# Kernel optimization log

Hardware: AMD Instinct MI355X
Metric: run time of the kernel (lower is better)

## Reference

```python
import jax, jax.numpy as jnp
import numpy as np


def setup_inputs() -> dict:
    key = jax.random.key(0)
    ks = jax.random.split(key, 9)
    B, T, C, H = 4, 2048, 1024, 16
    hd = C // H  # 64
    s = 0.02
    return {
        "x": jax.random.normal(ks[0], (B, T, C), dtype=jnp.float32),
        "Wq": jax.random.normal(ks[1], (H, C, hd), dtype=jnp.float32) * s,
        "bq": jax.random.normal(ks[2], (H, hd), dtype=jnp.float32) * s,
        "Wk": jax.random.normal(ks[3], (H, C, hd), dtype=jnp.float32) * s,
        "bk": jax.random.normal(ks[4], (H, hd), dtype=jnp.float32) * s,
        "Wv": jax.random.normal(ks[5], (H, C, hd), dtype=jnp.float32) * s,
        "bv": jax.random.normal(ks[6], (H, hd), dtype=jnp.float32) * s,
        "Wp": jax.random.normal(ks[7], (C, C), dtype=jnp.float32) * s,
        "bp": jax.random.normal(ks[8], (C,), dtype=jnp.float32) * s,
    }


def reference(x, Wq, bq, Wk, bk, Wv, bv, Wp, bp):
    B, T, C = x.shape
    # per-head projections, batched over heads: [B,H,T,hd]
    q = jnp.einsum('btc,hcd->bhtd', x, Wq) + bq[None, :, None, :]
    k = jnp.einsum('btc,hcd->bhtd', x, Wk) + bk[None, :, None, :]
    v = jnp.einsum('btc,hcd->bhtd', x, Wv) + bv[None, :, None, :]
    # NOTE: original scales by full embed dim C (not head_size) -- faithful quirk
    scale = jnp.asarray(C, x.dtype) ** -0.5
    wei = jnp.einsum('bhtd,bhsd->bhts', q, k) * scale  # [B,H,T,T]
    causal = jnp.tril(jnp.ones((T, T), dtype=bool))
    wei = jnp.where(causal, wei, jnp.asarray(-jnp.inf, wei.dtype))
    wei = jax.nn.softmax(wei, axis=-1)
    out = jnp.einsum('bhts,bhsd->bhtd', wei, v)  # [B,H,T,hd]
    # concat heads along feature dim -> [B,T,C]
    out = out.transpose(0, 2, 1, 3).reshape(B, T, C)
    return out @ Wp + bp
```

## Files before the change

### kernel.cpp

```cpp
#include <hip/hip_runtime.h>
#include <hip/hip_bf16.h>
#include <stdint.h>


typedef unsigned short u16;
typedef __attribute__((ext_vector_type(4))) float f32x4;
typedef __attribute__((ext_vector_type(8))) __bf16 bf16x8;
typedef __attribute__((ext_vector_type(2))) __bf16 bf16x2;

#define DEV static __device__ __forceinline__

DEV u16 f2bf(float f) {
  uint32_t u = __builtin_bit_cast(uint32_t, f);
  return (u16)((u + 0x7FFFu + ((u >> 16) & 1u)) >> 16);
}

DEV uint pack2(float a, float b) {
  bf16x2 v;
  v.x = (__bf16)a;
  v.y = (__bf16)b;
  return __builtin_bit_cast(uint, v);
}

#if __has_builtin(__builtin_amdgcn_exp2f)
DEV float fexp2(float x) { return __builtin_amdgcn_exp2f(x); }
#else
DEV float fexp2(float x) { return __expf(x * 0.69314718056f); }
#endif

DEV void gload_lds16(const void* g, void* lds) {
  auto gp = reinterpret_cast<const __attribute__((address_space(1))) uint32_t*>(
      reinterpret_cast<uintptr_t>(g));
  auto lp = reinterpret_cast<__attribute__((address_space(3))) uint32_t*>(
      static_cast<uint32_t>(reinterpret_cast<uintptr_t>(lds)));
  __builtin_amdgcn_global_load_lds(gp, lp, 16, 0, 0);
}

DEV f32x4 mfma16(bf16x8 a, bf16x8 b, f32x4 c) {
  return __builtin_amdgcn_mfma_f32_16x16x32_bf16(a, b, c, 0, 0, 0);
}

DEV void bar() {
  asm volatile("" ::: "memory");
  __builtin_amdgcn_s_barrier();
  asm volatile("" ::: "memory");
}

#define LD8(p) (*reinterpret_cast<const bf16x8*>(p))
#define LDU4(p) (*reinterpret_cast<const uint4*>(p))


__global__ void cvt_x_kernel(const float* __restrict__ x, u16* __restrict__ xb, int n8) {
  int i = blockIdx.x * blockDim.x + threadIdx.x;
  int stride = gridDim.x * blockDim.x;
  for (; i < n8; i += stride) {
    const float4* xp = reinterpret_cast<const float4*>(x) + 2 * (size_t)i;
    float4 a = xp[0], b = xp[1];
    uint4 o;
    o.x = pack2(a.x, a.y);
    o.y = pack2(a.z, a.w);
    o.z = pack2(b.x, b.y);
    o.w = pack2(b.z, b.w);
    reinterpret_cast<uint4*>(xb)[i] = o;
  }
}

__global__ void cvt_wqkv_kernel(const float* __restrict__ Wq, const float* __restrict__ Wk,
                                const float* __restrict__ Wv, const float* __restrict__ bq,
                                const float* __restrict__ bk, const float* __restrict__ bv,
                                u16* __restrict__ wt, float* __restrict__ biasq) {
  __shared__ u16 tle[64 * 72];
  const int tid = threadIdx.x;
  const int ct = blockIdx.x;
  const int h = blockIdx.y;
  const int which = blockIdx.z;
  const float* W = (which == 0) ? Wq : (which == 1) ? Wk : Wv;
  const float* Bb = (which == 0) ? bq : (which == 1) ? bk : bv;
  const float scl = (which == 0) ? 0.045084220027780106f : 1.0f;
#pragma unroll
  for (int i = 0; i < 4; ++i) {
    int idx = i * 256 + tid;
    int c_l = idx >> 4, d4 = (idx & 15) * 4;
    float4 v = *reinterpret_cast<const float4*>(&W[((size_t)(h * 1024 + ct * 64 + c_l)) * 64 + d4]);
    tle[(d4 + 0) * 72 + c_l] = f2bf(v.x * scl);
    tle[(d4 + 1) * 72 + c_l] = f2bf(v.y * scl);
    tle[(d4 + 2) * 72 + c_l] = f2bf(v.z * scl);
    tle[(d4 + 3) * 72 + c_l] = f2bf(v.w * scl);
  }
  __syncthreads();
#pragma unroll
  for (int i = 0; i < 2; ++i) {
    int idx = i * 256 + tid;
    int d_o = idx >> 3, c8 = (idx & 7) * 8;
    uint4 v = LDU4(&tle[d_o * 72 + c8]);
    *reinterpret_cast<uint4*>(&wt[(size_t)(which * 1024 + h * 64 + d_o) * 1024 + ct * 64 + c8]) = v;
  }
  if (ct == 0 && tid < 64) biasq[which * 1024 + h * 64 + tid] = Bb[h * 64 + tid] * scl;
}

__global__ void cvt_wp_kernel(const float* __restrict__ Wp, u16* __restrict__ wpt) {
  __shared__ u16 tle[64 * 72];
  const int tid = threadIdx.x;
  const int ct = blockIdx.x;
  const int nt = blockIdx.y;
#pragma unroll
  for (int i = 0; i < 4; ++i) {
    int idx = i * 256 + tid;
    int c_l = idx >> 4, n4 = (idx & 15) * 4;
    float4 v = *reinterpret_cast<const float4*>(&Wp[(size_t)(ct * 64 + c_l) * 1024 + nt * 64 + n4]);
    tle[(n4 + 0) * 72 + c_l] = f2bf(v.x);
    tle[(n4 + 1) * 72 + c_l] = f2bf(v.y);
    tle[(n4 + 2) * 72 + c_l] = f2bf(v.z);
    tle[(n4 + 3) * 72 + c_l] = f2bf(v.w);
  }
  __syncthreads();
#pragma unroll
  for (int i = 0; i < 2; ++i) {
    int idx = i * 256 + tid;
    int n_o = idx >> 3, c8 = (idx & 7) * 8;
    uint4 v = LDU4(&tle[n_o * 72 + c8]);
    *reinterpret_cast<uint4*>(&wpt[(size_t)(nt * 64 + n_o) * 1024 + ct * 64 + c8]) = v;
  }
}

__global__ __launch_bounds__(256)
void transpose_v_kernel(const u16* __restrict__ qkv, u16* __restrict__ vT) {
  __shared__ alignas(16) u16 tle[64 * 72];
  const int tid = threadIdx.x;
  const int tt = blockIdx.x;
  const int h = blockIdx.y;
  const int bb = blockIdx.z;
  const size_t rbase = ((size_t)bb * 2048 + tt * 64) * 3072 + 2048 + h * 64;
#pragma unroll
  for (int i = 0; i < 2; ++i) {
    int idx = i * 256 + tid;
    int s = idx >> 3, c8 = (idx & 7) * 8;
    *reinterpret_cast<uint4*>(&tle[s * 72 + c8]) = LDU4(&qkv[rbase + (size_t)s * 3072 + c8]);
  }
  __syncthreads();
#pragma unroll
  for (int i = 0; i < 2; ++i) {
    int idx = i * 256 + tid;
    int d = idx >> 3, cb = idx & 7;
    uint4 o;
    o.x = (uint)tle[(2 * cb + 0) * 72 + d] | ((uint)tle[(16 + 2 * cb + 0) * 72 + d] << 16);
    o.y = (uint)tle[(32 + 2 * cb + 0) * 72 + d] | ((uint)tle[(48 + 2 * cb + 0) * 72 + d] << 16);
    o.z = (uint)tle[(2 * cb + 1) * 72 + d] | ((uint)tle[(16 + 2 * cb + 1) * 72 + d] << 16);
    o.w = (uint)tle[(32 + 2 * cb + 1) * 72 + d] | ((uint)tle[(48 + 2 * cb + 1) * 72 + d] << 16);
    *reinterpret_cast<uint4*>(
        &vT[((size_t)(bb * 16 + h) * 64 + d) * 2048 + tt * 64 + cb * 8]) = o;
  }
}


template <bool OUT_F32>
__global__ __launch_bounds__(512, 4)
void gemm13_kernel(const u16* __restrict__ A, const u16* __restrict__ Bt,
                   const float* __restrict__ bias, void* __restrict__ Cout,
                   int M, int N, int K, int nbn) {
  __shared__ alignas(16) u16 LA[2 * 4096];
  __shared__ alignas(16) u16 LB[2 * 8192];

  const int tid = threadIdx.x;
  const int lane = tid & 63;
  const int wave = tid >> 6;
  const int wm = wave >> 2;
  const int wn = wave & 3;
  const int fr = lane & 15;
  const int kg = lane >> 4;
  const int r4 = kg * 4;

  const int nwg = gridDim.x;
  const int swz = (blockIdx.x & 7) * (nwg >> 3) + (blockIdx.x >> 3);
  const int m0 = (swz / nbn) * 128;
  const int n0 = (swz % nbn) * 256;
  const int NT = K >> 5;

  const int srow = tid >> 2;
  const int sgcol = (((tid & 3) ^ ((srow >> 1) & 3)) << 3);
  const size_t aOff = (size_t)(m0 + srow) * K + sgcol;
  const size_t bOff = (size_t)(n0 + srow) * K + sgcol;
  const int ldst = tid * 8;

  auto stageA = [&](int kt, u16* d) {
    gload_lds16(A + aOff + (size_t)kt * 32, d + ldst);
  };
  auto stageB = [&](int kt, u16* d) {
    gload_lds16(Bt + bOff + (size_t)kt * 32, d + ldst);
    gload_lds16(Bt + bOff + (size_t)128 * K + (size_t)kt * 32, d + 4096 + ldst);
  };

  f32x4 acc[4][4] = {};

  stageA(0, LA);
  stageB(0, LB);
  asm volatile("s_waitcnt vmcnt(0)" ::: "memory");
  bar();

  for (int kt = 0; kt < NT; ++kt) {
    const bool st1 = (kt + 1 < NT);
    u16* la = LA + (kt & 1) * 4096;
    u16* lb = LB + (kt & 1) * 8192;

    if (st1) {
      stageA(kt + 1, LA + ((kt + 1) & 1) * 4096);
      stageB(kt + 1, LB + ((kt + 1) & 1) * 8192);
    }

    bf16x8 aF[4], bF[4];
#pragma unroll
    for (int m = 0; m < 4; ++m) {
      const int R = wm * 64 + m * 16 + fr;
      aF[m] = LD8(&la[R * 32 + ((kg ^ ((R >> 1) & 3)) << 3)]);
    }
#pragma unroll
    for (int n = 0; n < 4; ++n) {
      const int R = wn * 64 + n * 16 + fr;
      bF[n] = LD8(&lb[R * 32 + ((kg ^ ((R >> 1) & 3)) << 3)]);
    }

    __builtin_amdgcn_s_setprio(1);
#pragma unroll
    for (int m = 0; m < 4; ++m)
#pragma unroll
      for (int n = 0; n < 4; ++n)
        acc[m][n] = mfma16(aF[m], bF[n], acc[m][n]);
    __builtin_amdgcn_s_setprio(0);

    if (st1) {
      asm volatile("s_waitcnt vmcnt(0)" ::: "memory");
      bar();
    }
  }

#pragma unroll
  for (int m = 0; m < 4; ++m) {
    const int row = m0 + wm * 64 + m * 16 + r4;
#pragma unroll
    for (int n = 0; n < 4; ++n) {
      const int col = n0 + wn * 64 + n * 16 + fr;
      const float bv = bias[col];
#pragma unroll
      for (int r = 0; r < 4; ++r) {
        float v = acc[m][n][r] + bv;
        size_t off = (size_t)(row + r) * N + col;
        if constexpr (OUT_F32) reinterpret_cast<float*>(Cout)[off] = v;
        else                   reinterpret_cast<u16*>(Cout)[off] = f2bf(v);
      }
    }
  }
}


template <bool OUT_F32>
__global__ __launch_bounds__(512, 2)
void gemm9_kernel(const u16* __restrict__ A, const u16* __restrict__ Bt,
                  const float* __restrict__ bias, void* __restrict__ Cout,
                  int M, int N, int K, int nbn) {
  __shared__ alignas(16) u16 LA[2 * 8192];
  __shared__ alignas(16) u16 LB[3 * 16384];

  const int tid = threadIdx.x;
  const int lane = tid & 63;
  const int wave = tid >> 6;
  const int wm = wave >> 2;
  const int wn = wave & 3;
  const int fr = lane & 15;
  const int kg = lane >> 4;
  const int f7 = fr & 7;
  const int r4 = kg * 4;

  const int nwg = gridDim.x;
  const int swz = (blockIdx.x & 7) * (nwg >> 3) + (blockIdx.x >> 3);
  const int m0 = (swz / nbn) * 128;
  const int n0 = (swz % nbn) * 256;
  const int NT = K >> 6;

  const int srow = tid >> 3;
  const int sgcol = ((tid & 7) ^ (srow & 7)) << 3;
  const size_t aOff = (size_t)(m0 + srow) * K + sgcol;
  const size_t bOff = (size_t)(n0 + srow) * K + sgcol;
  const int ldst = tid * 8;

  auto stageA = [&](int kt, u16* labuf) {
    gload_lds16(A + aOff + (size_t)kt * 64, labuf + ldst);
    gload_lds16(A + aOff + (size_t)64 * K + (size_t)kt * 64, labuf + 4096 + ldst);
  };
  auto stageB = [&](int kt, u16* lbbuf) {
    gload_lds16(Bt + bOff + (size_t)kt * 64, lbbuf + ldst);
    gload_lds16(Bt + bOff + (size_t)64 * K + (size_t)kt * 64, lbbuf + 4096 + ldst);
    gload_lds16(Bt + bOff + (size_t)128 * K + (size_t)kt * 64, lbbuf + 8192 + ldst);
    gload_lds16(Bt + bOff + (size_t)192 * K + (size_t)kt * 64, lbbuf + 12288 + ldst);
  };

  f32x4 acc[4][4] = {};

  stageA(0, LA);
  stageB(0, LB);
  if (NT > 1) {
    stageB(1, LB + 16384);
    asm volatile("s_waitcnt vmcnt(4)" ::: "memory");
  } else {
    asm volatile("s_waitcnt vmcnt(0)" ::: "memory");
  }
  bar();

  for (int kt = 0; kt < NT; ++kt) {
    const bool st1 = (kt + 1 < NT);
    const bool st2 = (kt + 2 < NT);
    u16* laCur = LA + (kt & 1) * 8192;
    u16* lbCur = LB + (kt % 3) * 16384;

    if (st1) stageA(kt + 1, LA + ((kt + 1) & 1) * 8192);
    if (st2) stageB(kt + 2, LB + ((kt + 2) % 3) * 16384);

    bf16x8 aF[4][2], bF[4][2];
#pragma unroll
    for (int m = 0; m < 4; ++m)
#pragma unroll
      for (int ks = 0; ks < 2; ++ks)
        aF[m][ks] = LD8(&laCur[wm * 4096 + (m * 16 + fr) * 64 + (((ks * 4 + kg) ^ f7) << 3)]);
#pragma unroll
    for (int n = 0; n < 4; ++n)
#pragma unroll
      for (int ks = 0; ks < 2; ++ks)
        bF[n][ks] = LD8(&lbCur[wn * 4096 + (n * 16 + fr) * 64 + (((ks * 4 + kg) ^ f7) << 3)]);

    __builtin_amdgcn_s_setprio(1);
#pragma unroll
    for (int ks = 0; ks < 2; ++ks)
#pragma unroll
      for (int m = 0; m < 4; ++m)
#pragma unroll
        for (int n = 0; n < 4; ++n)
          acc[m][n] = mfma16(aF[m][ks], bF[n][ks], acc[m][n]);
    __builtin_amdgcn_s_setprio(0);

    if (st1) {
      if (st2) asm volatile("s_waitcnt vmcnt(4)" ::: "memory");
      else     asm volatile("s_waitcnt vmcnt(0)" ::: "memory");
      bar();
    }
  }

#pragma unroll
  for (int m = 0; m < 4; ++m) {
    const int row = m0 + wm * 64 + m * 16 + r4;
#pragma unroll
    for (int n = 0; n < 4; ++n) {
      const int col = n0 + wn * 64 + n * 16 + fr;
      const float bv = bias[col];
#pragma unroll
      for (int r = 0; r < 4; ++r) {
        float v = acc[m][n][r] + bv;
        size_t off = (size_t)(row + r) * N + col;
        if constexpr (OUT_F32) reinterpret_cast<float*>(Cout)[off] = v;
        else                   reinterpret_cast<u16*>(Cout)[off] = f2bf(v);
      }
    }
  }
}


__global__ __launch_bounds__(128)
void attn_kernel(const u16* __restrict__ qkv, const u16* __restrict__ vT,
                 u16* __restrict__ obuf) {
  __shared__ alignas(16) u16 Ks[2][64 * 64];
  __shared__ alignas(16) u16 Vs[2][64 * 64];
  __shared__ alignas(16) u16 Ps[2][64 * 72];

  const int tid = threadIdx.x;
  const int lane = tid & 63;
  const int wave = tid >> 6;

  const int gid = blockIdx.x;
  const int xcd = gid & 7;
  const int j = gid >> 3;
  const int g = xcd * 8 + (j >> 3);
  const int pair = j & 7;
  const int bb = g >> 4;
  const int h = g & 15;

  const size_t baseQ = (size_t)bb * 2048 * 3072 + h * 64;
  const size_t baseK = baseQ + 1024;
  const size_t baseVt = (size_t)(bb * 16 + h) * 64 * 2048;

  const int fr = lane & 15;
  const int kg = lane >> 4;
  const int kg8 = kg * 8;
  const int r4 = kg * 4;
  const int f7 = fr & 7;
  const int ko0 = (kg ^ f7) * 8;
  const int ko1 = ((4 + kg) ^ f7) * 8;
  u16* __restrict__ Pw = &Ps[wave][0];

  auto stageKV = [&](int t, int bi) {
    const u16* kS = qkv + baseK + (size_t)t * 64 * 3072;
    const u16* vS = vT + baseVt + (size_t)t * 64;
#pragma unroll
    for (int i = 0; i < 4; ++i) {
      const int c = i * 128 + tid;
      const int rr = c >> 3;
      const int ss = ((c & 7) ^ (rr & 7)) * 8;
      gload_lds16(kS + (size_t)rr * 3072 + ss, &Ks[bi][c * 8]);
      gload_lds16(vS + (size_t)rr * 2048 + ss, &Vs[bi][c * 8]);
    }
  };

  for (int half = 0; half < 2; ++half) {
    const int qt = half ? (15 - pair) : pair;
    const int q0 = qt * 128;
    const int nt = 2 * qt + 2;
    const int myNt = nt - 1 + wave;
    const int qw = wave * 64;

    const u16* qr = &qkv[baseQ + (size_t)(q0 + qw + fr) * 3072 + kg8];
    bf16x8 aq00 = LD8(qr), aq01 = LD8(qr + 32);
    bf16x8 aq10 = LD8(qr + 16 * 3072), aq11 = LD8(qr + 16 * 3072 + 32);
    bf16x8 aq20 = LD8(qr + 32 * 3072), aq21 = LD8(qr + 32 * 3072 + 32);
    bf16x8 aq30 = LD8(qr + 48 * 3072), aq31 = LD8(qr + 48 * 3072 + 32);

    float ls00 = 0.f, ls01 = 0.f, ls02 = 0.f, ls03 = 0.f;
    float ls10 = 0.f, ls11 = 0.f, ls12 = 0.f, ls13 = 0.f;
    float ls20 = 0.f, ls21 = 0.f, ls22 = 0.f, ls23 = 0.f;
    float ls30 = 0.f, ls31 = 0.f, ls32 = 0.f, ls33 = 0.f;
    f32x4 o00 = {}, o01 = {}, o02 = {}, o03 = {};
    f32x4 o10 = {}, o11 = {}, o12 = {}, o13 = {};
    f32x4 o20 = {}, o21 = {}, o22 = {}, o23 = {};
    f32x4 o30 = {}, o31 = {}, o32 = {}, o33 = {};

    stageKV(0, 0);
    asm volatile("s_waitcnt vmcnt(0)" ::: "memory");
    bar();

    for (int t = 0; t < nt; ++t) {
      if (t + 1 < nt) stageKV(t + 1, (t + 1) & 1);

      if (t < myNt) {
        const u16* ks = &Ks[t & 1][0];
        const u16* vs = &Vs[t & 1][0];

        f32x4 s00 = {}, s01 = {}, s02 = {}, s03 = {};
        f32x4 s10 = {}, s11 = {}, s12 = {}, s13 = {};
        f32x4 s20 = {}, s21 = {}, s22 = {}, s23 = {};
        f32x4 s30 = {}, s31 = {}, s32 = {}, s33 = {};
        {
          bf16x8 b;
          __builtin_amdgcn_s_setprio(1);
          b = LD8(&ks[(fr) * 64 + ko0]);      s00 = mfma16(aq00, b, s00); s10 = mfma16(aq10, b, s10); s20 = mfma16(aq20, b, s20); s30 = mfma16(aq30, b, s30);
          b = LD8(&ks[(16 + fr) * 64 + ko0]); s01 = mfma16(aq00, b, s01); s11 = mfma16(aq10, b, s11); s21 = mfma16(aq20, b, s21); s31 = mfma16(aq30, b, s31);
          b = LD8(&ks[(32 + fr) * 64 + ko0]); s02 = mfma16(aq00, b, s02); s12 = mfma16(aq10, b, s12); s22 = mfma16(aq20, b, s22); s32 = mfma16(aq30, b, s32);
          b = LD8(&ks[(48 + fr) * 64 + ko0]); s03 = mfma16(aq00, b, s03); s13 = mfma16(aq10, b, s13); s23 = mfma16(aq20, b, s23); s33 = mfma16(aq30, b, s33);
          b = LD8(&ks[(fr) * 64 + ko1]);      s00 = mfma16(aq01, b, s00); s10 = mfma16(aq11, b, s10); s20 = mfma16(aq21, b, s20); s30 = mfma16(aq31, b, s30);
          b = LD8(&ks[(16 + fr) * 64 + ko1]); s01 = mfma16(aq01, b, s01); s11 = mfma16(aq11, b, s11); s21 = mfma16(aq21, b, s21); s31 = mfma16(aq31, b, s31);
          b = LD8(&ks[(32 + fr) * 64 + ko1]); s02 = mfma16(aq01, b, s02); s12 = mfma16(aq11, b, s12); s22 = mfma16(aq21, b, s22); s32 = mfma16(aq31, b, s32);
          b = LD8(&ks[(48 + fr) * 64 + ko1]); s03 = mfma16(aq01, b, s03); s13 = mfma16(aq11, b, s13); s23 = mfma16(aq21, b, s23); s33 = mfma16(aq31, b, s33);
          __builtin_amdgcn_s_setprio(0);
        }

        const bool diag = (t == myNt - 1);
#define SM_ROW(G, r, Sa, Sb, Sc, Sd, LS)                                       \
        {                                                                      \
          const int qgl = G * 16 + r4 + r;                                     \
          float p0 = fexp2(Sa[r]);                                             \
          float p1 = fexp2(Sb[r]);                                             \
          float p2 = fexp2(Sc[r]);                                             \
          float p3 = fexp2(Sd[r]);                                             \
          if (diag) {                                                          \
            if (fr > qgl) p0 = 0.f;                                            \
            if (fr + 16 > qgl) p1 = 0.f;                                       \
            if (fr + 32 > qgl) p2 = 0.f;                                       \
            if (fr + 48 > qgl) p3 = 0.f;                                       \
          }                                                                    \
          LS += (p0 + p1) + (p2 + p3);                                         \
          uint2 w;                                                             \
          w.x = pack2(p0, p1);                                                 \
          w.y = pack2(p2, p3);                                                 \
          *reinterpret_cast<uint2*>(&Pw[(G * 16 + r4 + r) * 72 + fr * 4]) = w; \
        }
        SM_ROW(0, 0, s00, s01, s02, s03, ls00)
        SM_ROW(0, 1, s00, s01, s02, s03, ls01)
        SM_ROW(0, 2, s00, s01, s02, s03, ls02)
        SM_ROW(0, 3, s00, s01, s02, s03, ls03)
        SM_ROW(1, 0, s10, s11, s12, s13, ls10)
        SM_ROW(1, 1, s10, s11, s12, s13, ls11)
        SM_ROW(1, 2, s10, s11, s12, s13, ls12)
        SM_ROW(1, 3, s10, s11, s12, s13, ls13)
        SM_ROW(2, 0, s20, s21, s22, s23, ls20)
        SM_ROW(2, 1, s20, s21, s22, s23, ls21)
        SM_ROW(2, 2, s20, s21, s22, s23, ls22)
        SM_ROW(2, 3, s20, s21, s22, s23, ls23)
        SM_ROW(3, 0, s30, s31, s32, s33, ls30)
        SM_ROW(3, 1, s30, s31, s32, s33, ls31)
        SM_ROW(3, 2, s30, s31, s32, s33, ls32)
        SM_ROW(3, 3, s30, s31, s32, s33, ls33)
#undef SM_ROW

        {
          bf16x8 v;
          __builtin_amdgcn_s_setprio(1);
          bf16x8 pf0 = LD8(&Pw[(fr) * 72 + kg8]);
          bf16x8 pf1 = LD8(&Pw[(16 + fr) * 72 + kg8]);
          bf16x8 pf2 = LD8(&Pw[(32 + fr) * 72 + kg8]);
          bf16x8 pf3 = LD8(&Pw[(48 + fr) * 72 + kg8]);
          v = LD8(&vs[(fr) * 64 + ko0]);      o00 = mfma16(pf0, v, o00); o10 = mfma16(pf1, v, o10); o20 = mfma16(pf2, v, o20); o30 = mfma16(pf3, v, o30);
          v = LD8(&vs[(16 + fr) * 64 + ko0]); o01 = mfma16(pf0, v, o01); o11 = mfma16(pf1, v, o11); o21 = mfma16(pf2, v, o21); o31 = mfma16(pf3, v, o31);
          v = LD8(&vs[(32 + fr) * 64 + ko0]); o02 = mfma16(pf0, v, o02); o12 = mfma16(pf1, v, o12); o22 = mfma16(pf2, v, o22); o32 = mfma16(pf3, v, o32);
          v = LD8(&vs[(48 + fr) * 64 + ko0]); o03 = mfma16(pf0, v, o03); o13 = mfma16(pf1, v, o13); o23 = mfma16(pf2, v, o23); o33 = mfma16(pf3, v, o33);
          pf0 = LD8(&Pw[(fr) * 72 + 32 + kg8]);
          pf1 = LD8(&Pw[(16 + fr) * 72 + 32 + kg8]);
          pf2 = LD8(&Pw[(32 + fr) * 72 + 32 + kg8]);
          pf3 = LD8(&Pw[(48 + fr) * 72 + 32 + kg8]);
          v = LD8(&vs[(fr) * 64 + ko1]);      o00 = mfma16(pf0, v, o00); o10 = mfma16(pf1, v, o10); o20 = mfma16(pf2, v, o20); o30 = mfma16(pf3, v, o30);
          v = LD8(&vs[(16 + fr) * 64 + ko1]); o01 = mfma16(pf0, v, o01); o11 = mfma16(pf1, v, o11); o21 = mfma16(pf2, v, o21); o31 = mfma16(pf3, v, o31);
          v = LD8(&vs[(32 + fr) * 64 + ko1]); o02 = mfma16(pf0, v, o02); o12 = mfma16(pf1, v, o12); o22 = mfma16(pf2, v, o22); o32 = mfma16(pf3, v, o32);
          v = LD8(&vs[(48 + fr) * 64 + ko1]); o03 = mfma16(pf0, v, o03); o13 = mfma16(pf1, v, o13); o23 = mfma16(pf2, v, o23); o33 = mfma16(pf3, v, o33);
          __builtin_amdgcn_s_setprio(0);
        }
      }

      if (t + 1 < nt) asm volatile("s_waitcnt vmcnt(0)" ::: "memory");
      bar();
    }

#define EPI(G, r, O0, O1, O2, O3, LS)                                          \
    {                                                                          \
      float s = LS;                                                            \
      s += __shfl_xor(s, 1);                                                   \
      s += __shfl_xor(s, 2);                                                   \
      s += __shfl_xor(s, 4);                                                   \
      s += __shfl_xor(s, 8);                                                   \
      const float inv = 1.0f / s;                                              \
      const int qg = q0 + qw + G * 16 + r4 + r;                                \
      const size_t rowoff = ((size_t)bb * 2048 + qg) * 1024 + h * 64;          \
      obuf[rowoff + fr] = f2bf(O0[r] * inv);                                   \
      obuf[rowoff + 16 + fr] = f2bf(O1[r] * inv);                              \
      obuf[rowoff + 32 + fr] = f2bf(O2[r] * inv);                              \
      obuf[rowoff + 48 + fr] = f2bf(O3[r] * inv);                              \
    }
    EPI(0, 0, o00, o01, o02, o03, ls00)
    EPI(0, 1, o00, o01, o02, o03, ls01)
    EPI(0, 2, o00, o01, o02, o03, ls02)
    EPI(0, 3, o00, o01, o02, o03, ls03)
    EPI(1, 0, o10, o11, o12, o13, ls10)
    EPI(1, 1, o10, o11, o12, o13, ls11)
    EPI(1, 2, o10, o11, o12, o13, ls12)
    EPI(1, 3, o10, o11, o12, o13, ls13)
    EPI(2, 0, o20, o21, o22, o23, ls20)
    EPI(2, 1, o20, o21, o22, o23, ls21)
    EPI(2, 2, o20, o21, o22, o23, ls22)
    EPI(2, 3, o20, o21, o22, o23, ls23)
    EPI(3, 0, o30, o31, o32, o33, ls30)
    EPI(3, 1, o30, o31, o32, o33, ls31)
    EPI(3, 2, o30, o31, o32, o33, ls32)
    EPI(3, 3, o30, o31, o32, o33, ls33)
#undef EPI
  }
}


extern "C" void kernel_launch(void* const* d_in, const int* in_sizes, int n_in,
                              void* d_out, int out_size, void* d_ws, size_t ws_size,
                              hipStream_t stream) {
  const float* x  = (const float*)d_in[0];
  const float* Wq = (const float*)d_in[1];
  const float* bq = (const float*)d_in[2];
  const float* Wk = (const float*)d_in[3];
  const float* bk = (const float*)d_in[4];
  const float* Wv = (const float*)d_in[5];
  const float* bv = (const float*)d_in[6];
  const float* Wp = (const float*)d_in[7];
  const float* bp = (const float*)d_in[8];

  char* ws = (char*)d_ws;
  size_t off = 0;
  auto alloc = [&](size_t bytes) -> void* {
    void* p = ws + off;
    off += (bytes + 255) & ~(size_t)255;
    return p;
  };
  u16*   xb     = (u16*)  alloc((size_t)8192 * 1024 * 2);
  u16*   wqkv_t = (u16*)  alloc((size_t)3072 * 1024 * 2);
  float* biasq  = (float*)alloc((size_t)3072 * 4);
  u16*   wpt    = (u16*)  alloc((size_t)1024 * 1024 * 2);
  u16*   qkv    = (u16*)  alloc((size_t)8192 * 3072 * 2);
  u16*   obuf   = (u16*)  alloc((size_t)8192 * 1024 * 2);
  u16*   vT     = xb;
  (void)ws_size; (void)in_sizes; (void)n_in; (void)out_size;

  cvt_x_kernel<<<2048, 256, 0, stream>>>(x, xb, 8192 * 1024 / 8);
  cvt_wqkv_kernel<<<dim3(16, 16, 3), 256, 0, stream>>>(Wq, Wk, Wv, bq, bk, bv, wqkv_t, biasq);
  cvt_wp_kernel<<<dim3(16, 16), 256, 0, stream>>>(Wp, wpt);
  gemm13_kernel<false><<<768, 512, 0, stream>>>(xb, wqkv_t, biasq, qkv, 8192, 3072, 1024, 12);
  transpose_v_kernel<<<dim3(32, 16, 4), 256, 0, stream>>>(qkv, vT);
  attn_kernel<<<512, 128, 0, stream>>>(qkv, vT, obuf);
  gemm9_kernel<true><<<256, 512, 0, stream>>>(obuf, wpt, bp, d_out, 8192, 1024, 1024, 4);
}
```

Measured before the change: 172.1 us.

## Split attention block into four 32-row waves to cut per-wave registers

The attention kernel now runs 256 threads (4 waves), each wave handling 32 query rows instead of 64, with per-wave P buffers resized and K/V staging spread across more threads. This halves the per-wave score and output accumulator register footprint and targets more resident waves per CU (launch bounds 256,3) to hide latency. In exchange each wave does fewer MFMAs per K/V fragment loaded from LDS, so LDS read traffic per flop rises.

```diff
diff --git a/kernel.cpp b/kernel.cpp
--- a/kernel.cpp
+++ b/kernel.cpp
@@ -362,12 +362,12 @@
 }
 
 
-__global__ __launch_bounds__(128)
+__global__ __launch_bounds__(256, 3)
 void attn_kernel(const u16* __restrict__ qkv, const u16* __restrict__ vT,
                  u16* __restrict__ obuf) {
   __shared__ alignas(16) u16 Ks[2][64 * 64];
   __shared__ alignas(16) u16 Vs[2][64 * 64];
-  __shared__ alignas(16) u16 Ps[2][64 * 72];
+  __shared__ alignas(16) u16 Ps[4][32 * 72];
 
   const int tid = threadIdx.x;
   const int lane = tid & 63;
@@ -398,8 +398,8 @@
     const u16* kS = qkv + baseK + (size_t)t * 64 * 3072;
     const u16* vS = vT + baseVt + (size_t)t * 64;
 #pragma unroll
-    for (int i = 0; i < 4; ++i) {
-      const int c = i * 128 + tid;
+    for (int i = 0; i < 2; ++i) {
+      const int c = i * 256 + tid;
       const int rr = c >> 3;
       const int ss = ((c & 7) ^ (rr & 7)) * 8;
       gload_lds16(kS + (size_t)rr * 3072 + ss, &Ks[bi][c * 8]);
@@ -411,23 +411,18 @@
     const int qt = half ? (15 - pair) : pair;
     const int q0 = qt * 128;
     const int nt = 2 * qt + 2;
-    const int myNt = nt - 1 + wave;
-    const int qw = wave * 64;
+    const int qw = wave * 32;
+    const int myNt = nt - 1 + (wave >> 1);
+    const int qdb = qw & 63;
 
     const u16* qr = &qkv[baseQ + (size_t)(q0 + qw + fr) * 3072 + kg8];
     bf16x8 aq00 = LD8(qr), aq01 = LD8(qr + 32);
     bf16x8 aq10 = LD8(qr + 16 * 3072), aq11 = LD8(qr + 16 * 3072 + 32);
-    bf16x8 aq20 = LD8(qr + 32 * 3072), aq21 = LD8(qr + 32 * 3072 + 32);
-    bf16x8 aq30 = LD8(qr + 48 * 3072), aq31 = LD8(qr + 48 * 3072 + 32);
-
-    float ls00 = 0.f, ls01 = 0.f, ls02 = 0.f, ls03 = 0.f;
-    float ls10 = 0.f, ls11 = 0.f, ls12 = 0.f, ls13 = 0.f;
-    float ls20 = 0.f, ls21 = 0.f, ls22 = 0.f, ls23 = 0.f;
-    float ls30 = 0.f, ls31 = 0.f, ls32 = 0.f, ls33 = 0.f;
-    f32x4 o00 = {}, o01 = {}, o02 = {}, o03 = {};
-    f32x4 o10 = {}, o11 = {}, o12 = {}, o13 = {};
-    f32x4 o20 = {}, o21 = {}, o22 = {}, o23 = {};
-    f32x4 o30 = {}, o31 = {}, o32 = {}, o33 = {};
+
+    float lsA0 = 0.f, lsA1 = 0.f, lsA2 = 0.f, lsA3 = 0.f;
+    float lsB0 = 0.f, lsB1 = 0.f, lsB2 = 0.f, lsB3 = 0.f;
+    f32x4 oA0 = {}, oA1 = {}, oA2 = {}, oA3 = {};
+    f32x4 oB0 = {}, oB1 = {}, oB2 = {}, oB3 = {};
 
     stageKV(0, 0);
     asm volatile("s_waitcnt vmcnt(0)" ::: "memory");
@@ -440,81 +435,67 @@
         const u16* ks = &Ks[t & 1][0];
         const u16* vs = &Vs[t & 1][0];
 
-        f32x4 s00 = {}, s01 = {}, s02 = {}, s03 = {};
-        f32x4 s10 = {}, s11 = {}, s12 = {}, s13 = {};
-        f32x4 s20 = {}, s21 = {}, s22 = {}, s23 = {};
-        f32x4 s30 = {}, s31 = {}, s32 = {}, s33 = {};
+        f32x4 sA0 = {}, sA1 = {}, sA2 = {}, sA3 = {};
+        f32x4 sB0 = {}, sB1 = {}, sB2 = {}, sB3 = {};
         {
           bf16x8 b;
           __builtin_amdgcn_s_setprio(1);
-          b = LD8(&ks[(fr) * 64 + ko0]);      s00 = mfma16(aq00, b, s00); s10 = mfma16(aq10, b, s10); s20 = mfma16(aq20, b, s20); s30 = mfma16(aq30, b, s30);
-          b = LD8(&ks[(16 + fr) * 64 + ko0]); s01 = mfma16(aq00, b, s01); s11 = mfma16(aq10, b, s11); s21 = mfma16(aq20, b, s21); s31 = mfma16(aq30, b, s31);
-          b = LD8(&ks[(32 + fr) * 64 + ko0]); s02 = mfma16(aq00, b, s02); s12 = mfma16(aq10, b, s12); s22 = mfma16(aq20, b, s22); s32 = mfma16(aq30, b, s32);
-          b = LD8(&ks[(48 + fr) * 64 + ko0]); s03 = mfma16(aq00, b, s03); s13 = mfma16(aq10, b, s13); s23 = mfma16(aq20, b, s23); s33 = mfma16(aq30, b, s33);
-          b = LD8(&ks[(fr) * 64 + ko1]);      s00 = mfma16(aq01, b, s00); s10 = mfma16(aq11, b, s10); s20 = mfma16(aq21, b, s20); s30 = mfma16(aq31, b, s30);
-          b = LD8(&ks[(16 + fr) * 64 + ko1]); s01 = mfma16(aq01, b, s01); s11 = mfma16(aq11, b, s11); s21 = mfma16(aq21, b, s21); s31 = mfma16(aq31, b, s31);
-          b = LD8(&ks[(32 + fr) * 64 + ko1]); s02 = mfma16(aq01, b, s02); s12 = mfma16(aq11, b, s12); s22 = mfma16(aq21, b, s22); s32 = mfma16(aq31, b, s32);
-          b = LD8(&ks[(48 + fr) * 64 + ko1]); s03 = mfma16(aq01, b, s03); s13 = mfma16(aq11, b, s13); s23 = mfma16(aq21, b, s23); s33 = mfma16(aq31, b, s33);
+          b = LD8(&ks[(fr) * 64 + ko0]);      sA0 = mfma16(aq00, b, sA0); sB0 = mfma16(aq10, b, sB0);
+          b = LD8(&ks[(16 + fr) * 64 + ko0]); sA1 = mfma16(aq00, b, sA1); sB1 = mfma16(aq10, b, sB1);
+          b = LD8(&ks[(32 + fr) * 64 + ko0]); sA2 = mfma16(aq00, b, sA2); sB2 = mfma16(aq10, b, sB2);
+          b = LD8(&ks[(48 + fr) * 64 + ko0]); sA3 = mfma16(aq00, b, sA3); sB3 = mfma16(aq10, b, sB3);
+          b = LD8(&ks[(fr) * 64 + ko1]);      sA0 = mfma16(aq01, b, sA0); sB0 = mfma16(aq11, b, sB0);
+          b = LD8(&ks[(16 + fr) * 64 + ko1]); sA1 = mfma16(aq01, b, sA1); sB1 = mfma16(aq11, b, sB1);
+          b = LD8(&ks[(32 + fr) * 64 + ko1]); sA2 = mfma16(aq01, b, sA2); sB2 = mfma16(aq11, b, sB2);
+          b = LD8(&ks[(48 + fr) * 64 + ko1]); sA3 = mfma16(aq01, b, sA3); sB3 = mfma16(aq11, b, sB3);
           __builtin_amdgcn_s_setprio(0);
         }
 
         const bool diag = (t == myNt - 1);
-#define SM_ROW(G, r, Sa, Sb, Sc, Sd, LS)                                       \
+#define SM_ROW_G(S0, S1, S2, S3, LS, RB, r)                                    \
         {                                                                      \
-          const int qgl = G * 16 + r4 + r;                                     \
-          float p0 = fexp2(Sa[r]);                                             \
-          float p1 = fexp2(Sb[r]);                                             \
-          float p2 = fexp2(Sc[r]);                                             \
-          float p3 = fexp2(Sd[r]);                                             \
+          const int qd = qdb + RB + r4 + r;                                    \
+          float p0 = fexp2(S0[r]);                                             \
+          float p1 = fexp2(S1[r]);                                             \
+          float p2 = fexp2(S2[r]);                                             \
+          float p3 = fexp2(S3[r]);                                             \
           if (diag) {                                                          \
-            if (fr > qgl) p0 = 0.f;                                            \
-            if (fr + 16 > qgl) p1 = 0.f;                                       \
-            if (fr + 32 > qgl) p2 = 0.f;                                       \
-            if (fr + 48 > qgl) p3 = 0.f;                                       \
+            if (fr > qd) p0 = 0.f;                                             \
+            if (fr + 16 > qd) p1 = 0.f;                                        \
+            if (fr + 32 > qd) p2 = 0.f;                                        \
+            if (fr + 48 > qd) p3 = 0.f;                                        \
           }                                                                    \
           LS += (p0 + p1) + (p2 + p3);                                         \
           uint2 w;                                                             \
           w.x = pack2(p0, p1);                                                 \
           w.y = pack2(p2, p3);                                                 \
-          *reinterpret_cast<uint2*>(&Pw[(G * 16 + r4 + r) * 72 + fr * 4]) = w; \
+          *reinterpret_cast<uint2*>(&Pw[(RB + r4 + r) * 72 + fr * 4]) = w;     \
         }
-        SM_ROW(0, 0, s00, s01, s02, s03, ls00)
-        SM_ROW(0, 1, s00, s01, s02, s03, ls01)
-        SM_ROW(0, 2, s00, s01, s02, s03, ls02)
-        SM_ROW(0, 3, s00, s01, s02, s03, ls03)
-        SM_ROW(1, 0, s10, s11, s12, s13, ls10)
-        SM_ROW(1, 1, s10, s11, s12, s13, ls11)
-        SM_ROW(1, 2, s10, s11, s12, s13, ls12)
-        SM_ROW(1, 3, s10, s11, s12, s13, ls13)
-        SM_ROW(2, 0, s20, s21, s22, s23, ls20)
-        SM_ROW(2, 1, s20, s21, s22, s23, ls21)
-        SM_ROW(2, 2, s20, s21, s22, s23, ls22)
-        SM_ROW(2, 3, s20, s21, s22, s23, ls23)
-        SM_ROW(3, 0, s30, s31, s32, s33, ls30)
-        SM_ROW(3, 1, s30, s31, s32, s33, ls31)
-        SM_ROW(3, 2, s30, s31, s32, s33, ls32)
-        SM_ROW(3, 3, s30, s31, s32, s33, ls33)
-#undef SM_ROW
+        SM_ROW_G(sA0, sA1, sA2, sA3, lsA0, 0, 0)
+        SM_ROW_G(sA0, sA1, sA2, sA3, lsA1, 0, 1)
+        SM_ROW_G(sA0, sA1, sA2, sA3, lsA2, 0, 2)
+        SM_ROW_G(sA0, sA1, sA2, sA3, lsA3, 0, 3)
+        SM_ROW_G(sB0, sB1, sB2, sB3, lsB0, 16, 0)
+        SM_ROW_G(sB0, sB1, sB2, sB3, lsB1, 16, 1)
+        SM_ROW_G(sB0, sB1, sB2, sB3, lsB2, 16, 2)
+        SM_ROW_G(sB0, sB1, sB2, sB3, lsB3, 16, 3)
+#undef SM_ROW_G
 
         {
+          bf16x8 pfA = LD8(&Pw[fr * 72 + kg8]);
+          bf16x8 pfB = LD8(&Pw[(16 + fr) * 72 + kg8]);
           bf16x8 v;
           __builtin_amdgcn_s_setprio(1);
-          bf16x8 pf0 = LD8(&Pw[(fr) * 72 + kg8]);
-          bf16x8 pf1 = LD8(&Pw[(16 + fr) * 72 + kg8]);
-          bf16x8 pf2 = LD8(&Pw[(32 + fr) * 72 + kg8]);
-          bf16x8 pf3 = LD8(&Pw[(48 + fr) * 72 + kg8]);
-          v = LD8(&vs[(fr) * 64 + ko0]);      o00 = mfma16(pf0, v, o00); o10 = mfma16(pf1, v, o10); o20 = mfma16(pf2, v, o20); o30 = mfma16(pf3, v, o30);
-          v = LD8(&vs[(16 + fr) * 64 + ko0]); o01 = mfma16(pf0, v, o01); o11 = mfma16(pf1, v, o11); o21 = mfma16(pf2, v, o21); o31 = mfma16(pf3, v, o31);
-          v = LD8(&vs[(32 + fr) * 64 + ko0]); o02 = mfma16(pf0, v, o02); o12 = mfma16(pf1, v, o12); o22 = mfma16(pf2, v, o22); o32 = mfma16(pf3, v, o32);
-          v = LD8(&vs[(48 + fr) * 64 + ko0]); o03 = mfma16(pf0, v, o03); o13 = mfma16(pf1, v, o13); o23 = mfma16(pf2, v, o23); o33 = mfma16(pf3, v, o33);
-          pf0 = LD8(&Pw[(fr) * 72 + 32 + kg8]);
-          pf1 = LD8(&Pw[(16 + fr) * 72 + 32 + kg8]);
-          pf2 = LD8(&Pw[(32 + fr) * 72 + 32 + kg8]);
-          pf3 = LD8(&Pw[(48 + fr) * 72 + 32 + kg8]);
-          v = LD8(&vs[(fr) * 64 + ko1]);      o00 = mfma16(pf0, v, o00); o10 = mfma16(pf1, v, o10); o20 = mfma16(pf2, v, o20); o30 = mfma16(pf3, v, o30);
-          v = LD8(&vs[(16 + fr) * 64 + ko1]); o01 = mfma16(pf0, v, o01); o11 = mfma16(pf1, v, o11); o21 = mfma16(pf2, v, o21); o31 = mfma16(pf3, v, o31);
-          v = LD8(&vs[(32 + fr) * 64 + ko1]); o02 = mfma16(pf0, v, o02); o12 = mfma16(pf1, v, o12); o22 = mfma16(pf2, v, o22); o32 = mfma16(pf3, v, o32);
-          v = LD8(&vs[(48 + fr) * 64 + ko1]); o03 = mfma16(pf0, v, o03); o13 = mfma16(pf1, v, o13); o23 = mfma16(pf2, v, o23); o33 = mfma16(pf3, v, o33);
+          v = LD8(&vs[(fr) * 64 + ko0]);      oA0 = mfma16(pfA, v, oA0); oB0 = mfma16(pfB, v, oB0);
+          v = LD8(&vs[(16 + fr) * 64 + ko0]); oA1 = mfma16(pfA, v, oA1); oB1 = mfma16(pfB, v, oB1);
+          v = LD8(&vs[(32 + fr) * 64 + ko0]); oA2 = mfma16(pfA, v, oA2); oB2 = mfma16(pfB, v, oB2);
+          v = LD8(&vs[(48 + fr) * 64 + ko0]); oA3 = mfma16(pfA, v, oA3); oB3 = mfma16(pfB, v, oB3);
+          pfA = LD8(&Pw[fr * 72 + 32 + kg8]);
+          pfB = LD8(&Pw[(16 + fr) * 72 + 32 + kg8]);
+          v = LD8(&vs[(fr) * 64 + ko1]);      oA0 = mfma16(pfA, v, oA0); oB0 = mfma16(pfB, v, oB0);
+          v = LD8(&vs[(16 + fr) * 64 + ko1]); oA1 = mfma16(pfA, v, oA1); oB1 = mfma16(pfB, v, oB1);
+          v = LD8(&vs[(32 + fr) * 64 + ko1]); oA2 = mfma16(pfA, v, oA2); oB2 = mfma16(pfB, v, oB2);
+          v = LD8(&vs[(48 + fr) * 64 + ko1]); oA3 = mfma16(pfA, v, oA3); oB3 = mfma16(pfB, v, oB3);
           __builtin_amdgcn_s_setprio(0);
         }
       }
@@ -523,7 +504,7 @@
       bar();
     }
 
-#define EPI(G, r, O0, O1, O2, O3, LS)                                          \
+#define EPI_G(O0, O1, O2, O3, LS, RB, r)                                       \
     {                                                                          \
       float s = LS;                                                            \
       s += __shfl_xor(s, 1);                                                   \
@@ -531,30 +512,22 @@
       s += __shfl_xor(s, 4);                                                   \
       s += __shfl_xor(s, 8);                                                   \
       const float inv = 1.0f / s;                                              \
-      const int qg = q0 + qw + G * 16 + r4 + r;                                \
+      const int qg = q0 + qw + RB + r4 + r;                                    \
       const size_t rowoff = ((size_t)bb * 2048 + qg) * 1024 + h * 64;          \
       obuf[rowoff + fr] = f2bf(O0[r] * inv);                                   \
       obuf[rowoff + 16 + fr] = f2bf(O1[r] * inv);                              \
       obuf[rowoff + 32 + fr] = f2bf(O2[r] * inv);                              \
       obuf[rowoff + 48 + fr] = f2bf(O3[r] * inv);                              \
     }
-    EPI(0, 0, o00, o01, o02, o03, ls00)
-    EPI(0, 1, o00, o01, o02, o03, ls01)
-    EPI(0, 2, o00, o01, o02, o03, ls02)
-    EPI(0, 3, o00, o01, o02, o03, ls03)
-    EPI(1, 0, o10, o11, o12, o13, ls10)
-    EPI(1, 1, o10, o11, o12, o13, ls11)
-    EPI(1, 2, o10, o11, o12, o13, ls12)
-    EPI(1, 3, o10, o11, o12, o13, ls13)
-    EPI(2, 0, o20, o21, o22, o23, ls20)
-    EPI(2, 1, o20, o21, o22, o23, ls21)
-    EPI(2, 2, o20, o21, o22, o23, ls22)
-    EPI(2, 3, o20, o21, o22, o23, ls23)
-    EPI(3, 0, o30, o31, o32, o33, ls30)
-    EPI(3, 1, o30, o31, o32, o33, ls31)
-    EPI(3, 2, o30, o31, o32, o33, ls32)
-    EPI(3, 3, o30, o31, o32, o33, ls33)
-#undef EPI
+    EPI_G(oA0, oA1, oA2, oA3, lsA0, 0, 0)
+    EPI_G(oA0, oA1, oA2, oA3, lsA1, 0, 1)
+    EPI_G(oA0, oA1, oA2, oA3, lsA2, 0, 2)
+    EPI_G(oA0, oA1, oA2, oA3, lsA3, 0, 3)
+    EPI_G(oB0, oB1, oB2, oB3, lsB0, 16, 0)
+    EPI_G(oB0, oB1, oB2, oB3, lsB1, 16, 1)
+    EPI_G(oB0, oB1, oB2, oB3, lsB2, 16, 2)
+    EPI_G(oB0, oB1, oB2, oB3, lsB3, 16, 3)
+#undef EPI_G
   }
 }
 
@@ -593,6 +566,6 @@
   cvt_wp_kernel<<<dim3(16, 16), 256, 0, stream>>>(Wp, wpt);
   gemm13_kernel<false><<<768, 512, 0, stream>>>(xb, wqkv_t, biasq, qkv, 8192, 3072, 1024, 12);
   transpose_v_kernel<<<dim3(32, 16, 4), 256, 0, stream>>>(qkv, vT);
-  attn_kernel<<<512, 128, 0, stream>>>(qkv, vT, obuf);
+  attn_kernel<<<512, 256, 0, stream>>>(qkv, vT, obuf);
   gemm9_kernel<true><<<256, 512, 0, stream>>>(obuf, wpt, bp, d_out, 8192, 1024, 1024, 4);
 }
```

After: 157.6 us. -8.4%, faster.
